# Kernel optimization log

Hardware: AMD Instinct MI355X
Metric: run time of the kernel (lower is better)

## Reference

```python
import jax, jax.numpy as jnp
import numpy as np

N = 50000      # nodes
E = 800000     # edges (avg degree 16)
IN = 256       # input feature dim
HID = 128      # hidden dim
H = 4          # heads
C = HID // H   # per-head dim = 32
L = 3          # layers


def setup_inputs() -> dict:
    key = jax.random.key(0)
    ks = jax.random.split(key, 16)
    s = 0.02
    f32 = jnp.float32
    inp = {
        "x": jax.random.normal(ks[0], (N, IN), f32),
        "edge_index": jax.random.randint(ks[1], (2, E), 0, N, dtype=jnp.int32),
        "edge_attr": jax.random.normal(ks[2], (E, 1), f32),
        "Wi": jax.random.normal(ks[3], (IN, HID), f32) * s,
        "bi": jnp.zeros((HID,), f32),
        "Wq": jax.random.normal(ks[4], (L, HID, HID), f32) * s,
        "bq": jnp.zeros((L, HID), f32),
        "Wk": jax.random.normal(ks[5], (L, HID, HID), f32) * s,
        "bk": jnp.zeros((L, HID), f32),
        "Wv": jax.random.normal(ks[6], (L, HID, HID), f32) * s,
        "bv": jnp.zeros((L, HID), f32),
        "We": jax.random.normal(ks[7], (L, 1, HID), f32) * s,      # lin_edge, no bias
        "Wskip": jax.random.normal(ks[8], (L, HID, HID), f32) * s,
        "bskip": jnp.zeros((L, HID), f32),
        "Wbeta": jax.random.normal(ks[9], (L, 3 * HID, 1), f32) * s,  # lin_beta, no bias
        "ln_g": jnp.ones((L, HID), f32),
        "ln_b": jnp.zeros((L, HID), f32),
    }
    return inp


def _layer_norm(x, g, b, eps=1e-5):
    mu = jnp.mean(x, axis=-1, keepdims=True)
    var = jnp.var(x, axis=-1, keepdims=True)
    return (x - mu) * jax.lax.rsqrt(var + eps) * g + b


def _transformer_conv(h, src, dst, edge_attr, Wq, bq, Wk, bk, Wv, bv, We, Wskip, bskip, Wbeta):
    # node-level projections [N, HID]
    q = h @ Wq + bq
    k = h @ Wk + bk
    v = h @ Wv + bv
    e = edge_attr @ We                       # [E, HID] edge embedding
    # per-edge gathered features [E, H, C]
    qi = q[dst].reshape(E, H, C)
    kj = (k[src] + e).reshape(E, H, C)
    vj = (v[src] + e).reshape(E, H, C)
    # attention logits [E, H]
    alpha = jnp.sum(qi * kj, axis=-1) / np.sqrt(C)
    # segment softmax over destination node
    amax = jax.ops.segment_max(alpha, dst, num_segments=N)   # [N, H]
    ex = jnp.exp(alpha - amax[dst])
    denom = jax.ops.segment_sum(ex, dst, num_segments=N)     # [N, H]
    attn = ex / (denom[dst] + 1e-16)                         # [E, H]
    # scatter-add aggregation -> [N, H, C] -> concat heads [N, HID]
    out = jax.ops.segment_sum(attn[..., None] * vj, dst, num_segments=N).reshape(N, HID)
    # gated skip (beta=True, root_weight=True)
    x_r = h @ Wskip + bskip
    beta = jax.nn.sigmoid(jnp.concatenate([out, x_r, out - x_r], axis=-1) @ Wbeta)  # [N, 1]
    return beta * x_r + (1.0 - beta) * out


def reference(x, edge_index, edge_attr, Wi, bi, Wq, bq, Wk, bk, Wv, bv, We, Wskip, bskip, Wbeta, ln_g, ln_b):
    src = edge_index[0]
    dst = edge_index[1]
    h = x @ Wi + bi
    for l in range(L):
        res = h
        h = _transformer_conv(h, src, dst, edge_attr,
                              Wq[l], bq[l], Wk[l], bk[l], Wv[l], bv[l],
                              We[l], Wskip[l], bskip[l], Wbeta[l])
        h = jax.nn.gelu(h, approximate=False)
        h = _layer_norm(h + res, ln_g[l], ln_b[l])
        # dropout: eval mode -> identity
    return h
```

## Files before the change

### kernel.cpp

```cpp
#include <hip/hip_runtime.h>
#include <math.h>

#define NNODES 50000
#define NEDGES 800000
#define DIN 256
#define DHID 128
#define GBLK 391
#define NBUCK 196
#define CHUNK 4096

typedef __attribute__((ext_vector_type(8))) short short8;
typedef __attribute__((ext_vector_type(4))) float f32x4;
typedef __attribute__((ext_vector_type(2))) float f32x2;

__device__ __forceinline__ unsigned short f2bf(float f) {
    unsigned u = __builtin_bit_cast(unsigned, f);
    u += 0x7fffu + ((u >> 16) & 1u);
    return (unsigned short)(u >> 16);
}
__device__ __forceinline__ float bf2f(unsigned short s) {
    return __builtin_bit_cast(float, (unsigned)s << 16);
}
__device__ __forceinline__ unsigned packbf(float a, float b) {
    return (unsigned)f2bf(a) | ((unsigned)f2bf(b) << 16);
}
__device__ __forceinline__ float dpp_xor1(float x) {
    return __builtin_bit_cast(float, __builtin_amdgcn_update_dpp(0, __builtin_bit_cast(int, x), 0xB1, 0xF, 0xF, true));
}
__device__ __forceinline__ float dpp_xor2(float x) {
    return __builtin_bit_cast(float, __builtin_amdgcn_update_dpp(0, __builtin_bit_cast(int, x), 0x4E, 0xF, 0xF, true));
}
__device__ __forceinline__ float dpp_hmirror(float x) {
    return __builtin_bit_cast(float, __builtin_amdgcn_update_dpp(0, __builtin_bit_cast(int, x), 0x141, 0xF, 0xF, true));
}
__device__ __forceinline__ float dpp_mirror(float x) {
    return __builtin_bit_cast(float, __builtin_amdgcn_update_dpp(0, __builtin_bit_cast(int, x), 0x140, 0xF, 0xF, true));
}
__device__ __forceinline__ float red16(float x) {
    x += dpp_xor1(x);
    x += dpp_xor2(x);
    x += dpp_hmirror(x);
    x += dpp_mirror(x);
    return x;
}

__global__ __launch_bounds__(256) void prep_hist(const float* __restrict__ Wi, const float* __restrict__ Wq,
                                                 const float* __restrict__ Wk, const float* __restrict__ Wv,
                                                 const float* __restrict__ Ws, unsigned short* __restrict__ Wit,
                                                 unsigned short* __restrict__ Wt3, const int* __restrict__ dst,
                                                 int* __restrict__ counts, int pb) {
    if ((int)blockIdx.x < pb) {
        int idx = blockIdx.x * 256 + threadIdx.x;
        if (idx < DHID * DIN) {
            int n = idx >> 8, kk = idx & 255;
            Wit[idx] = f2bf(Wi[kk * DHID + n]);
        }
        int idx2 = idx - DHID * DIN;
        if (idx2 >= 0 && idx2 < 3 * 512 * DHID) {
            int l = idx2 / (512 * DHID);
            int rem = idx2 - l * 512 * DHID;
            int r = rem >> 7;
            int kk = rem & 127;
            int sel = r >> 7, rl = r & 127;
            const float* srcm = sel == 0 ? Wq : sel == 1 ? Wk : sel == 2 ? Wv : Ws;
            Wt3[idx2] = f2bf(srcm[l * DHID * DHID + kk * DHID + rl]);
        }
    } else {
        int e = (blockIdx.x - pb) * 256 + threadIdx.x;
        if (e < NEDGES) atomicAdd(&counts[dst[e]], 1);
    }
}

__global__ __launch_bounds__(256) void k_scan_block(const int* __restrict__ in, int* __restrict__ out,
                                                    int* __restrict__ partials, int n, int* __restrict__ dh) {
    __shared__ int sh[256];
    __shared__ int dhist[256];
    int tid = threadIdx.x;
    int i = blockIdx.x * 256 + tid;
    int vv = (i < n) ? in[i] : 0;
    sh[tid] = vv;
    dhist[tid] = 0;
    __syncthreads();
    if (i < n) atomicAdd(&dhist[min(vv, 255)], 1);
    for (int off = 1; off < 256; off <<= 1) {
        int t = (tid >= off) ? sh[tid - off] : 0;
        __syncthreads();
        sh[tid] += t;
        __syncthreads();
    }
    if (i < n) out[i] = sh[tid];
    if (tid == 255) partials[blockIdx.x] = sh[255];
    __syncthreads();
    int hc = dhist[tid];
    if (hc) atomicAdd(&dh[tid], hc);
}

__global__ __launch_bounds__(256) void k_apply2(const int* __restrict__ partials, int* __restrict__ row_ptr, int n,
                                                int nb, const int* __restrict__ dh, int* __restrict__ dbase) {
    __shared__ int sh[256];
    int tid = threadIdx.x;
    int vv = (tid < nb) ? partials[tid] : 0;
    sh[tid] = vv;
    __syncthreads();
    for (int off = 1; off < 256; off <<= 1) {
        int t = (tid >= off) ? sh[tid - off] : 0;
        __syncthreads();
        sh[tid] += t;
        __syncthreads();
    }
    int i = blockIdx.x * 256 + tid;
    if (i < n) {
        int add = blockIdx.x ? sh[blockIdx.x - 1] : 0;
        row_ptr[i + 1] += add;
    }
    if (i == 0) row_ptr[0] = 0;
    if (blockIdx.x == 0) {
        __syncthreads();
        int c = dh[255 - tid];
        sh[tid] = c;
        __syncthreads();
        for (int off = 1; off < 256; off <<= 1) {
            int t = (tid >= off) ? sh[tid - off] : 0;
            __syncthreads();
            sh[tid] += t;
            __syncthreads();
        }
        dbase[255 - tid] = sh[tid] - c;
    }
}

__global__ __launch_bounds__(256) void perm_scatter(const int* __restrict__ counts, const int* __restrict__ dbase,
                                                    int* __restrict__ dfill, int* __restrict__ perm) {
    __shared__ int h[256], gb[256], c2[256];
    const int tid = threadIdx.x;
    int i = blockIdx.x * 256 + tid;
    int d = (i < NNODES) ? min(counts[i], 255) : -1;
    h[tid] = 0;
    c2[tid] = 0;
    __syncthreads();
    if (d >= 0) atomicAdd(&h[d], 1);
    __syncthreads();
    int c = h[tid];
    gb[tid] = c ? dbase[tid] + atomicAdd(&dfill[tid], c) : 0;
    __syncthreads();
    if (d >= 0) {
        int r = atomicAdd(&c2[d], 1);
        perm[gb[d] + r] = i;
    }
}

__global__ __launch_bounds__(256) void bin_edges(const int* __restrict__ src, const int* __restrict__ dst,
                                                 const float* __restrict__ ea, const int* __restrict__ row_ptr,
                                                 int* __restrict__ bfill, unsigned* __restrict__ brec,
                                                 unsigned char* __restrict__ bdst) {
    __shared__ int hist[NBUCK];
    __shared__ int lbase[NBUCK];
    __shared__ int gbase[NBUCK];
    __shared__ int cnt[NBUCK];
    __shared__ unsigned rec4[CHUNK];
    __shared__ unsigned char dl8[CHUNK];
    __shared__ unsigned char bk8[CHUNK];
    const int tid = threadIdx.x;
    const int e0 = blockIdx.x * CHUNK;
    const int n = min(NEDGES - e0, CHUNK);
    for (int i = tid; i < NBUCK; i += 256) hist[i] = 0;
    __syncthreads();
    for (int i = tid; i < n; i += 256) atomicAdd(&hist[dst[e0 + i] >> 8], 1);
    __syncthreads();
    if (tid == 0) {
        int run = 0;
        for (int b = 0; b < NBUCK; ++b) {
            lbase[b] = run;
            run += hist[b];
        }
    }
    __syncthreads();
    for (int b = tid; b < NBUCK; b += 256) {
        int h = hist[b];
        int off = h ? atomicAdd(&bfill[b], h) : 0;
        gbase[b] = row_ptr[b << 8] + off;
        cnt[b] = lbase[b];
    }
    __syncthreads();
    for (int i = tid; i < n; i += 256) {
        int d = dst[e0 + i];
        int b = d >> 8;
        int lp = atomicAdd(&cnt[b], 1);
        rec4[lp] = (unsigned)src[e0 + i] | ((unsigned)f2bf(ea[e0 + i]) << 16);
        dl8[lp] = (unsigned char)(d & 255);
        bk8[lp] = (unsigned char)b;
    }
    __syncthreads();
    for (int i = tid; i < n; i += 256) {
        int b = bk8[i];
        int pos = gbase[b] + (i - lbase[b]);
        brec[pos] = rec4[i];
        bdst[pos] = dl8[i];
    }
}

__global__ __launch_bounds__(256) void sort_bucket(const unsigned* __restrict__ brec,
                                                   const unsigned char* __restrict__ bdst,
                                                   const int* __restrict__ row_ptr, unsigned* __restrict__ esrc) {
    __shared__ int rp[257];
    __shared__ int cnt[256];
    const int b = blockIdx.x;
    const int d0 = b << 8;
    const int nmax = min(256, NNODES - d0);
    const int tid = threadIdx.x;
    for (int i = tid; i <= nmax; i += 256) rp[i] = row_ptr[d0 + i];
    cnt[tid] = 0;
    __syncthreads();
    const int base = rp[0], end = rp[nmax];
    for (int i = base + tid; i < end; i += 256) {
        unsigned rec = brec[i];
        int d = bdst[i];
        int rank = atomicAdd(&cnt[d], 1);
        esrc[rp[d] + rank] = rec;
    }
}

__global__ __launch_bounds__(256) void gemm_in(const float* __restrict__ A, const unsigned short* __restrict__ Wt,
                                               const float* __restrict__ bias, unsigned* __restrict__ h32, int M) {
    __shared__ short As[128 * 128];
    const int tid = threadIdx.x;
    const int lane = tid & 63;
    const int wid = tid >> 6;
    const int row0 = blockIdx.x * 128;
    const int wr = (wid & 1) * 64;
    const int wc = (wid >> 1) * 64;
    f32x4 acc[4][4] = {};
    const int srow = tid >> 1;
    const int sk = (tid & 1) * 64;
    const int grow = min(row0 + srow, M - 1);
    for (int kt = 0; kt < 2; ++kt) {
        const float* ap = A + (size_t)grow * DIN + kt * 128 + sk;
#pragma unroll
        for (int i = 0; i < 8; ++i) {
            float4 f0 = *(const float4*)(ap + i * 8);
            float4 f1 = *(const float4*)(ap + i * 8 + 4);
            short8 s;
            s[0] = f2bf(f0.x); s[1] = f2bf(f0.y); s[2] = f2bf(f0.z); s[3] = f2bf(f0.w);
            s[4] = f2bf(f1.x); s[5] = f2bf(f1.y); s[6] = f2bf(f1.z); s[7] = f2bf(f1.w);
            int g = (sk >> 3) + i;
            *(short8*)(&As[srow * 128 + ((g ^ (srow & 7)) << 3)]) = s;
        }
        __syncthreads();
#pragma unroll
        for (int ks = 0; ks < 4; ++ks) {
            short8 a[4], b[4];
#pragma unroll
            for (int m = 0; m < 4; ++m) {
                int r = wr + m * 16 + (lane & 15);
                int g = ks * 4 + (lane >> 4);
                a[m] = *(const short8*)(&As[r * 128 + ((g ^ (r & 7)) << 3)]);
            }
#pragma unroll
            for (int n = 0; n < 4; ++n) {
                int c = wc + n * 16 + (lane & 15);
                b[n] = *(const short8*)(Wt + (size_t)c * DIN + kt * 128 + ks * 32 + (lane >> 4) * 8);
            }
#pragma unroll
            for (int m = 0; m < 4; ++m)
#pragma unroll
                for (int n = 0; n < 4; ++n)
                    acc[m][n] = __builtin_amdgcn_mfma_f32_16x16x32_bf16(a[m], b[n], acc[m][n], 0, 0, 0);
        }
        __syncthreads();
    }
    float* my = ((float*)As) + wid * 1024;
    float bb[4];
#pragma unroll
    for (int n = 0; n < 4; ++n) bb[n] = bias[wc + n * 16 + (lane & 15)];
    const int rr = lane >> 2;
    const int cb = lane & 3;
#pragma unroll
    for (int m = 0; m < 4; ++m) {
#pragma unroll
        for (int n = 0; n < 4; ++n) {
            int lc = n * 16 + (lane & 15);
#pragma unroll
            for (int j = 0; j < 4; ++j) {
                int row = (lane >> 4) * 4 + j;
                my[row * 64 + (((lc >> 2) ^ (row & 7)) << 2) + (lc & 3)] = acc[m][n][j] + bb[n];
            }
        }
        float vals[16];
#pragma unroll
        for (int s = 0; s < 4; ++s) {
            int gx = (cb * 4 + s) ^ (rr & 7);
            f32x4 t4 = *(const f32x4*)(my + rr * 64 + gx * 4);
            vals[s * 4 + 0] = t4.x; vals[s * 4 + 1] = t4.y; vals[s * 4 + 2] = t4.z; vals[s * 4 + 3] = t4.w;
        }
        int grow2 = row0 + wr + m * 16 + rr;
        if (grow2 < M) {
            unsigned pk[8];
#pragma unroll
            for (int d = 0; d < 8; ++d) pk[d] = packbf(vals[2 * d], vals[2 * d + 1]);
            unsigned* op = h32 + (size_t)grow2 * 64 + (wc >> 1) + cb * 8;
            *(uint4*)op = make_uint4(pk[0], pk[1], pk[2], pk[3]);
            *(uint4*)(op + 4) = make_uint4(pk[4], pk[5], pk[6], pk[7]);
        }
    }
}

__global__ __launch_bounds__(512) void gemm_qkvs(const unsigned short* __restrict__ A,
                                                 const unsigned short* __restrict__ Wt, const float* __restrict__ bq,
                                                 const float* __restrict__ bk, const float* __restrict__ bv,
                                                 const float* __restrict__ bs, unsigned* __restrict__ q32,
                                                 unsigned* __restrict__ kv, unsigned* __restrict__ xr32, int M) {
    __shared__ short As[128 * 128];
    const int tid = threadIdx.x;
    const int lane = tid & 63;
    const int wid = tid >> 6;
    const int row0 = blockIdx.x * 128;
    const int sel = wid >> 2;
    const int wr = (wid & 1) * 64;
    const int wc = ((wid >> 1) & 1) * 64;
    f32x4 acc0[4][4] = {}, acc1[4][4] = {};
    {
        const int srow = tid >> 2;
        const int sk = (tid & 3) * 32;
        const int grow = min(row0 + srow, M - 1);
        const unsigned short* ap = A + (size_t)grow * DHID + sk;
#pragma unroll
        for (int i = 0; i < 4; ++i) {
            short8 s = *(const short8*)(ap + i * 8);
            int g = (sk >> 3) + i;
            *(short8*)(&As[srow * 128 + ((g ^ (srow & 7)) << 3)]) = s;
        }
    }
    __syncthreads();
    const int b0base = sel ? 128 : 0;
    const int b1base = sel ? 256 : 384;
#pragma unroll
    for (int ks = 0; ks < 4; ++ks) {
        short8 a[4], b0[4], b1[4];
#pragma unroll
        for (int m = 0; m < 4; ++m) {
            int r = wr + m * 16 + (lane & 15);
            int g = ks * 4 + (lane >> 4);
            a[m] = *(const short8*)(&As[r * 128 + ((g ^ (r & 7)) << 3)]);
        }
#pragma unroll
        for (int n = 0; n < 4; ++n) {
            int rb = wc + n * 16 + (lane & 15);
            b0[n] = *(const short8*)(Wt + (size_t)(b0base + rb) * DHID + ks * 32 + (lane >> 4) * 8);
            b1[n] = *(const short8*)(Wt + (size_t)(b1base + rb) * DHID + ks * 32 + (lane >> 4) * 8);
        }
#pragma unroll
        for (int m = 0; m < 4; ++m)
#pragma unroll
            for (int n = 0; n < 4; ++n) {
                acc0[m][n] = __builtin_amdgcn_mfma_f32_16x16x32_bf16(a[m], b0[n], acc0[m][n], 0, 0, 0);
                acc1[m][n] = __builtin_amdgcn_mfma_f32_16x16x32_bf16(a[m], b1[n], acc1[m][n], 0, 0, 0);
            }
    }
    __syncthreads();
    float* my = ((float*)As) + wid * 1024;
    const float* bias0 = sel ? bk : bq;
    const float* bias1 = sel ? bv : bs;
    float bb0[4], bb1[4];
#pragma unroll
    for (int n = 0; n < 4; ++n) {
        int c = wc + n * 16 + (lane & 15);
        bb0[n] = bias0[c];
        bb1[n] = bias1[c];
    }
    const int rr = lane >> 2;
    const int cb = lane & 3;
#pragma unroll
    for (int m = 0; m < 4; ++m) {
        float vals0[16], vals1[16];
#pragma unroll
        for (int n = 0; n < 4; ++n) {
            int lc = n * 16 + (lane & 15);
#pragma unroll
            for (int j = 0; j < 4; ++j) {
                int row = (lane >> 4) * 4 + j;
                my[row * 64 + (((lc >> 2) ^ (row & 7)) << 2) + (lc & 3)] = acc0[m][n][j] + bb0[n];
            }
        }
#pragma unroll
        for (int s = 0; s < 4; ++s) {
            int gx = (cb * 4 + s) ^ (rr & 7);
            f32x4 t4 = *(const f32x4*)(my + rr * 64 + gx * 4);
            vals0[s * 4 + 0] = t4.x; vals0[s * 4 + 1] = t4.y; vals0[s * 4 + 2] = t4.z; vals0[s * 4 + 3] = t4.w;
        }
#pragma unroll
        for (int n = 0; n < 4; ++n) {
            int lc = n * 16 + (lane & 15);
#pragma unroll
            for (int j = 0; j < 4; ++j) {
                int row = (lane >> 4) * 4 + j;
                my[row * 64 + (((lc >> 2) ^ (row & 7)) << 2) + (lc & 3)] = acc1[m][n][j] + bb1[n];
            }
        }
#pragma unroll
        for (int s = 0; s < 4; ++s) {
            int gx = (cb * 4 + s) ^ (rr & 7);
            f32x4 t4 = *(const f32x4*)(my + rr * 64 + gx * 4);
            vals1[s * 4 + 0] = t4.x; vals1[s * 4 + 1] = t4.y; vals1[s * 4 + 2] = t4.z; vals1[s * 4 + 3] = t4.w;
        }
        int grow2 = row0 + wr + m * 16 + rr;
        if (grow2 < M) {
            size_t obase = (size_t)grow2 * 64 + (wc >> 1) + cb * 8;
            if (sel == 0) {
                unsigned p0[8], p1[8];
#pragma unroll
                for (int d = 0; d < 8; ++d) {
                    p0[d] = packbf(vals0[2 * d], vals0[2 * d + 1]);
                    p1[d] = packbf(vals1[2 * d], vals1[2 * d + 1]);
                }
                *(uint4*)(q32 + obase) = make_uint4(p0[0], p0[1], p0[2], p0[3]);
                *(uint4*)(q32 + obase + 4) = make_uint4(p0[4], p0[5], p0[6], p0[7]);
                *(uint4*)(xr32 + obase) = make_uint4(p1[0], p1[1], p1[2], p1[3]);
                *(uint4*)(xr32 + obase + 4) = make_uint4(p1[4], p1[5], p1[6], p1[7]);
            } else {
                unsigned pk[8];
#pragma unroll
                for (int d = 0; d < 8; ++d) {
                    unsigned u = (unsigned)__builtin_amdgcn_cvt_pk_fp8_f32(vals0[2 * d], vals0[2 * d + 1], 0, false);
                    u = (unsigned)__builtin_amdgcn_cvt_pk_fp8_f32(vals1[2 * d], vals1[2 * d + 1], (int)u, true);
                    pk[d] = u;
                }
                *(uint4*)(kv + obase) = make_uint4(pk[0], pk[1], pk[2], pk[3]);
                *(uint4*)(kv + obase + 4) = make_uint4(pk[4], pk[5], pk[6], pk[7]);
            }
        }
    }
}

__global__ __launch_bounds__(256) void node_attn_fuse(const unsigned* __restrict__ q32,
                                                      const unsigned* __restrict__ kv, const unsigned* __restrict__ esrc,
                                                      const float* __restrict__ We, const int* __restrict__ row_ptr,
                                                      const int* __restrict__ perm, const unsigned* __restrict__ xr32,
                                                      const unsigned* res32, const float* __restrict__ Wb,
                                                      const float* __restrict__ lng, const float* __restrict__ lnb,
                                                      unsigned* houtb, float* houtf) {
    const int tid = threadIdx.x;
    const int lane = tid & 63;
    const int lnl = lane & 15;
    const int gbase = lane & 48;
    const int node = perm[blockIdx.x * 16 + (tid >> 4)];
    const int base = row_ptr[node], end = row_ptr[node + 1];
    const float SC = 0.25505654047688565f;
    const float THR = 8.0f;

    float qv[8], wev[8];
    {
        uint4 qw = *(const uint4*)(q32 + (size_t)node * 64 + 4 * lnl);
        unsigned qd[4] = {qw.x, qw.y, qw.z, qw.w};
#pragma unroll
        for (int t = 0; t < 4; ++t) {
            qv[2 * t] = bf2f((unsigned short)qd[t]) * SC;
            qv[2 * t + 1] = bf2f((unsigned short)(qd[t] >> 16)) * SC;
        }
        float4 wlo = *(const float4*)(We + 8 * lnl);
        float4 whi = *(const float4*)(We + 8 * lnl + 4);
        wev[0] = wlo.x; wev[1] = wlo.y; wev[2] = wlo.z; wev[3] = wlo.w;
        wev[4] = whi.x; wev[5] = whi.y; wev[6] = whi.z; wev[7] = whi.w;
    }
    float qwe;
    {
        float s = 0.f;
#pragma unroll
        for (int i = 0; i < 8; ++i) s = fmaf(qv[i], wev[i], s);
        s += dpp_xor1(s);
        s += dpp_xor2(s);
        qwe = s;
    }

    float m = -1e30f, sden = 0.f, tacc = 0.f;
    float acc[8] = {};
    const unsigned* kvp = kv + 4 * lnl;

    for (int off = 0; ; off += 16) {
        int cnt = min(end - base - off, 16);
        if (__all(cnt <= 0)) break;
        unsigned u_l = 0;
        if (lnl < cnt) u_l = esrc[base + off + lnl];
        int cm = max(cnt, 0);
        cm = max(cm, __shfl_xor(cm, 16));
        cm = max(cm, __shfl_xor(cm, 32));
        unsigned ueA[4], ueB[4];
        uint4 kwA[4], kwB[4];
#pragma unroll
        for (int s = 0; s < 4; ++s) {
            ueA[s] = (unsigned)__shfl((int)u_l, gbase + s);
            kwA[s] = *(const uint4*)(kvp + (size_t)(ueA[s] & 0xFFFFu) * 64);
        }
#pragma unroll
        for (int s = 0; s < 4; ++s) {
            ueB[s] = (unsigned)__shfl((int)u_l, gbase + 4 + s);
            kwB[s] = *(const uint4*)(kvp + (size_t)(ueB[s] & 0xFFFFu) * 64);
        }
        for (int j = 0; j < cm; j += 4) {
            float p[4], av[4];
#pragma unroll
            for (int s = 0; s < 4; ++s) {
                av[s] = bf2f((unsigned short)(ueA[s] >> 16));
                unsigned kd[4] = {kwA[s].x, kwA[s].y, kwA[s].z, kwA[s].w};
                float pp = 0.f;
#pragma unroll
                for (int t = 0; t < 4; ++t) {
                    f32x2 kk = __builtin_amdgcn_cvt_pk_f32_fp8((int)kd[t], false);
                    pp = fmaf(qv[2 * t], kk.x, pp);
                    pp = fmaf(qv[2 * t + 1], kk.y, pp);
                }
                p[s] = pp;
            }
#pragma unroll
            for (int s = 0; s < 4; ++s) {
                p[s] += dpp_xor1(p[s]);
                p[s] += dpp_xor2(p[s]);
                p[s] = fmaf(av[s], qwe, p[s]);
                p[s] = (j + s < cnt) ? p[s] : -3e38f;
            }
            float pm = fmaxf(fmaxf(p[0], p[1]), fmaxf(p[2], p[3]));
            float w[4];
            if (__any(pm - m > THR)) {
                float mn2 = fmaxf(m, pm);
                float sc = exp2f(m - mn2);
#pragma unroll
                for (int s = 0; s < 4; ++s) w[s] = exp2f(p[s] - mn2);
                sden = fmaf(sden, sc, (w[0] + w[1]) + (w[2] + w[3]));
                tacc = fmaf(tacc, sc, fmaf(w[0], av[0], w[1] * av[1]) + fmaf(w[2], av[2], w[3] * av[3]));
#pragma unroll
                for (int t = 0; t < 4; ++t) {
                    f32x2 v0 = __builtin_amdgcn_cvt_pk_f32_fp8((int)kwA[0].x, true);
                    (void)v0;
                }
#pragma unroll
                for (int i = 0; i < 8; ++i) acc[i] *= sc;
#pragma unroll
                for (int s = 0; s < 4; ++s) {
                    unsigned kd[4] = {kwA[s].x, kwA[s].y, kwA[s].z, kwA[s].w};
#pragma unroll
                    for (int t = 0; t < 4; ++t) {
                        f32x2 vv = __builtin_amdgcn_cvt_pk_f32_fp8((int)kd[t], true);
                        acc[2 * t] = fmaf(w[s], vv.x, acc[2 * t]);
                        acc[2 * t + 1] = fmaf(w[s], vv.y, acc[2 * t + 1]);
                    }
                }
                m = mn2;
            } else {
#pragma unroll
                for (int s = 0; s < 4; ++s) w[s] = exp2f(p[s] - m);
                sden += (w[0] + w[1]) + (w[2] + w[3]);
                tacc += fmaf(w[0], av[0], w[1] * av[1]) + fmaf(w[2], av[2], w[3] * av[3]);
#pragma unroll
                for (int s = 0; s < 4; ++s) {
                    unsigned kd[4] = {kwA[s].x, kwA[s].y, kwA[s].z, kwA[s].w};
#pragma unroll
                    for (int t = 0; t < 4; ++t) {
                        f32x2 vv = __builtin_amdgcn_cvt_pk_f32_fp8((int)kd[t], true);
                        acc[2 * t] = fmaf(w[s], vv.x, acc[2 * t]);
                        acc[2 * t + 1] = fmaf(w[s], vv.y, acc[2 * t + 1]);
                    }
                }
            }
#pragma unroll
            for (int s = 0; s < 4; ++s) {
                ueA[s] = ueB[s];
                kwA[s] = kwB[s];
            }
            if (j + 8 < cm) {
#pragma unroll
                for (int s = 0; s < 4; ++s) {
                    int slot = j + 8 + s;
                    slot = slot < 16 ? slot : 0;
                    ueB[s] = (unsigned)__shfl((int)u_l, gbase + slot);
                    kwB[s] = *(const uint4*)(kvp + (size_t)(ueB[s] & 0xFFFFu) * 64);
                }
            }
        }
    }

    float rden = 1.f / (sden + 1e-16f);
    float o[8];
#pragma unroll
    for (int i = 0; i < 8; ++i) o[i] = fmaf(tacc, wev[i], acc[i]) * rden;

    float x[8];
    {
        uint4 xw = *(const uint4*)(xr32 + (size_t)node * 64 + 4 * lnl);
        unsigned xd[4] = {xw.x, xw.y, xw.z, xw.w};
#pragma unroll
        for (int t = 0; t < 4; ++t) {
            x[2 * t] = bf2f((unsigned short)xd[t]);
            x[2 * t + 1] = bf2f((unsigned short)(xd[t] >> 16));
        }
    }
    float bl = 0.f;
#pragma unroll
    for (int t = 0; t < 2; ++t) {
        float4 w0 = *(const float4*)(Wb + 8 * lnl + 4 * t);
        float4 w1 = *(const float4*)(Wb + 128 + 8 * lnl + 4 * t);
        float4 w2 = *(const float4*)(Wb + 256 + 8 * lnl + 4 * t);
        bl = fmaf(o[4 * t], w0.x, bl); bl = fmaf(o[4 * t + 1], w0.y, bl);
        bl = fmaf(o[4 * t + 2], w0.z, bl); bl = fmaf(o[4 * t + 3], w0.w, bl);
        bl = fmaf(x[4 * t], w1.x, bl); bl = fmaf(x[4 * t + 1], w1.y, bl);
        bl = fmaf(x[4 * t + 2], w1.z, bl); bl = fmaf(x[4 * t + 3], w1.w, bl);
        bl = fmaf(o[4 * t] - x[4 * t], w2.x, bl); bl = fmaf(o[4 * t + 1] - x[4 * t + 1], w2.y, bl);
        bl = fmaf(o[4 * t + 2] - x[4 * t + 2], w2.z, bl); bl = fmaf(o[4 * t + 3] - x[4 * t + 3], w2.w, bl);
    }
    bl = red16(bl);
    float beta = 1.f / (1.f + __expf(-bl));
    float tpre[8];
    {
        uint4 rw = *(const uint4*)(res32 + (size_t)node * 64 + 4 * lnl);
        unsigned rd[4] = {rw.x, rw.y, rw.z, rw.w};
#pragma unroll
        for (int i = 0; i < 8; ++i) {
            float gg = beta * x[i] + (1.f - beta) * o[i];
            gg = 0.5f * gg * (1.f + erff(gg * 0.70710678118654752f));
            float rv = (i & 1) ? bf2f((unsigned short)(rd[i >> 1] >> 16)) : bf2f((unsigned short)rd[i >> 1]);
            tpre[i] = gg + rv;
        }
    }
    float su = 0.f, sq = 0.f;
#pragma unroll
    for (int i = 0; i < 8; ++i) {
        su += tpre[i];
        sq = fmaf(tpre[i], tpre[i], sq);
    }
    su = red16(su);
    sq = red16(sq);
    float mu = su * (1.f / 128.f);
    float var = sq * (1.f / 128.f) - mu * mu;
    float inv = rsqrtf(var + 1e-5f);
    float4 g0 = *(const float4*)(lng + 8 * lnl);
    float4 g1 = *(const float4*)(lng + 8 * lnl + 4);
    float4 b0 = *(const float4*)(lnb + 8 * lnl);
    float4 b1 = *(const float4*)(lnb + 8 * lnl + 4);
    float gg[8] = {g0.x, g0.y, g0.z, g0.w, g1.x, g1.y, g1.z, g1.w};
    float bb[8] = {b0.x, b0.y, b0.z, b0.w, b1.x, b1.y, b1.z, b1.w};
    float ov[8];
#pragma unroll
    for (int i = 0; i < 8; ++i) ov[i] = (tpre[i] - mu) * inv * gg[i] + bb[i];
    if (houtf) {
        float* op = houtf + (size_t)node * 128 + 8 * lnl;
        *(float4*)op = make_float4(ov[0], ov[1], ov[2], ov[3]);
        *(float4*)(op + 4) = make_float4(ov[4], ov[5], ov[6], ov[7]);
    } else {
        unsigned pk[4];
#pragma unroll
        for (int d = 0; d < 4; ++d) pk[d] = packbf(ov[2 * d], ov[2 * d + 1]);
        *(uint4*)(houtb + (size_t)node * 64 + 4 * lnl) = make_uint4(pk[0], pk[1], pk[2], pk[3]);
    }
}

extern "C" void kernel_launch(void* const* d_in, const int* in_sizes, int n_in, void* d_out, int out_size,
                              void* d_ws, size_t ws_size, hipStream_t stream) {
    const float* x = (const float*)d_in[0];
    const int* ei = (const int*)d_in[1];
    const float* ea = (const float*)d_in[2];
    const float* Wi = (const float*)d_in[3];
    const float* bi = (const float*)d_in[4];
    const float* Wq = (const float*)d_in[5];
    const float* bq = (const float*)d_in[6];
    const float* Wk = (const float*)d_in[7];
    const float* bk = (const float*)d_in[8];
    const float* Wv = (const float*)d_in[9];
    const float* bv = (const float*)d_in[10];
    const float* We = (const float*)d_in[11];
    const float* Wskip = (const float*)d_in[12];
    const float* bskip = (const float*)d_in[13];
    const float* Wbeta = (const float*)d_in[14];
    const float* lng = (const float*)d_in[15];
    const float* lnb = (const float*)d_in[16];

    const int* srcp = ei;
    const int* dstp = ei + NEDGES;

    char* p = (char*)d_ws;
    auto alloc = [&](size_t bytes) {
        void* r = (void*)p;
        p += (bytes + 255) & ~(size_t)255;
        return r;
    };
    unsigned* h32 = (unsigned*)alloc((size_t)NNODES * 64 * 4);
    unsigned* q32 = (unsigned*)alloc((size_t)NNODES * 64 * 4);
    unsigned* xr32 = (unsigned*)alloc((size_t)NNODES * 64 * 4);
    unsigned* kv = (unsigned*)alloc((size_t)NNODES * 64 * 4);
    unsigned short* Wit = (unsigned short*)alloc((size_t)DHID * DIN * 2);
    unsigned short* Wt3 = (unsigned short*)alloc((size_t)3 * 512 * DHID * 2);
    int* counts = (int*)alloc((size_t)(NNODES + 768) * 4);
    int* bfill = counts + NNODES;
    int* dh = bfill + 256;
    int* dfill = dh + 256;
    int* dbase = (int*)alloc(256 * 4);
    int* perm = (int*)alloc((size_t)NNODES * 4);
    int* row_ptr = (int*)alloc((size_t)(NNODES + 1) * 4);
    unsigned* esrc = (unsigned*)alloc((size_t)NEDGES * 4);
    unsigned* brec = (unsigned*)alloc((size_t)NEDGES * 4);
    unsigned char* bdst = (unsigned char*)alloc((size_t)NEDGES);
    int* partials = (int*)alloc(256 * 4);

    const int EB = (NEDGES + 255) / 256;
    const int NB = (NNODES + 255) / 256;
    const int WB = NNODES / 16;
    const int PB = (DHID * DIN + 3 * 512 * DHID + 255) / 256;
    const int AB = (NEDGES + CHUNK - 1) / CHUNK;

    hipMemsetAsync(counts, 0, (size_t)(NNODES + 768) * 4, stream);
    prep_hist<<<PB + EB, 256, 0, stream>>>(Wi, Wq, Wk, Wv, Wskip, Wit, Wt3, dstp, counts, PB);
    gemm_in<<<GBLK, 256, 0, stream>>>(x, Wit, bi, h32, NNODES);
    k_scan_block<<<NB, 256, 0, stream>>>(counts, row_ptr + 1, partials, NNODES, dh);
    k_apply2<<<NB, 256, 0, stream>>>(partials, row_ptr, NNODES, NB, dh, dbase);
    perm_scatter<<<NB, 256, 0, stream>>>(counts, dbase, dfill, perm);
    bin_edges<<<AB, 256, 0, stream>>>(srcp, dstp, ea, row_ptr, bfill, brec, bdst);
    sort_bucket<<<NBUCK, 256, 0, stream>>>(brec, bdst, row_ptr, esrc);

    for (int l = 0; l < 3; ++l) {
        const size_t bo = (size_t)l * 128;
        gemm_qkvs<<<GBLK, 512, 0, stream>>>((const unsigned short*)h32, Wt3 + (size_t)l * 512 * DHID, bq + bo, bk + bo,
                                            bv + bo, bskip + bo, q32, kv, xr32, NNODES);
        node_attn_fuse<<<WB, 256, 0, stream>>>(q32, kv, esrc, We + bo, row_ptr, perm, xr32, h32,
                                               Wbeta + (size_t)l * 384, lng + bo, lnb + bo, h32,
                                               (l == 2) ? (float*)d_out : nullptr);
    }
}
```

Baseline: 311.1 us.

## Split online softmax into two independent streams and merge perm/bin kernels

The attention loop now processes 8 edges per iteration as two independent online-softmax accumulators (X and Y), each with its own running max, denominator and accumulator, merged at the end. Loads for the next 8 edges are issued before the current ones are computed, which lengthens the prefetch distance and breaks the serial dependency on a single running max. Separately, the perm_scatter and bin_edges kernels are fused into one launch that branches on block index, saving a launch. The cost is higher register pressure from doubled accumulators and prefetch buffers, which could lower occupancy.

```diff
diff --git a/kernel.cpp b/kernel.cpp
--- a/kernel.cpp
+++ b/kernel.cpp
@@ -129,30 +129,12 @@
     }
 }
 
-__global__ __launch_bounds__(256) void perm_scatter(const int* __restrict__ counts, const int* __restrict__ dbase,
-                                                    int* __restrict__ dfill, int* __restrict__ perm) {
-    __shared__ int h[256], gb[256], c2[256];
-    const int tid = threadIdx.x;
-    int i = blockIdx.x * 256 + tid;
-    int d = (i < NNODES) ? min(counts[i], 255) : -1;
-    h[tid] = 0;
-    c2[tid] = 0;
-    __syncthreads();
-    if (d >= 0) atomicAdd(&h[d], 1);
-    __syncthreads();
-    int c = h[tid];
-    gb[tid] = c ? dbase[tid] + atomicAdd(&dfill[tid], c) : 0;
-    __syncthreads();
-    if (d >= 0) {
-        int r = atomicAdd(&c2[d], 1);
-        perm[gb[d] + r] = i;
-    }
-}
-
-__global__ __launch_bounds__(256) void bin_edges(const int* __restrict__ src, const int* __restrict__ dst,
-                                                 const float* __restrict__ ea, const int* __restrict__ row_ptr,
-                                                 int* __restrict__ bfill, unsigned* __restrict__ brec,
-                                                 unsigned char* __restrict__ bdst) {
+__global__ __launch_bounds__(256) void perm_bin(const int* __restrict__ counts, const int* __restrict__ dbase,
+                                                int* __restrict__ dfill, int* __restrict__ perm,
+                                                const int* __restrict__ src, const int* __restrict__ dst,
+                                                const float* __restrict__ ea, const int* __restrict__ row_ptr,
+                                                int* __restrict__ bfill, unsigned* __restrict__ brec,
+                                                unsigned char* __restrict__ bdst, int nb) {
     __shared__ int hist[NBUCK];
     __shared__ int lbase[NBUCK];
     __shared__ int gbase[NBUCK];
@@ -161,7 +143,27 @@
     __shared__ unsigned char dl8[CHUNK];
     __shared__ unsigned char bk8[CHUNK];
     const int tid = threadIdx.x;
-    const int e0 = blockIdx.x * CHUNK;
+    if ((int)blockIdx.x < nb) {
+        int* h = (int*)rec4;
+        int* gb = h + 256;
+        int* c2 = gb + 256;
+        int i = blockIdx.x * 256 + tid;
+        int d = (i < NNODES) ? min(counts[i], 255) : -1;
+        h[tid] = 0;
+        c2[tid] = 0;
+        __syncthreads();
+        if (d >= 0) atomicAdd(&h[d], 1);
+        __syncthreads();
+        int c = h[tid];
+        gb[tid] = c ? dbase[tid] + atomicAdd(&dfill[tid], c) : 0;
+        __syncthreads();
+        if (d >= 0) {
+            int r = atomicAdd(&c2[d], 1);
+            perm[gb[d] + r] = i;
+        }
+        return;
+    }
+    const int e0 = (blockIdx.x - nb) * CHUNK;
     const int n = min(NEDGES - e0, CHUNK);
     for (int i = tid; i < NBUCK; i += 256) hist[i] = 0;
     __syncthreads();
@@ -471,11 +473,11 @@
         qwe = s;
     }
 
-    float m = -1e30f, sden = 0.f, tacc = 0.f;
-    float acc[8] = {};
+    float mX = -1e30f, sdX = 0.f, taX = 0.f, accX[8] = {};
+    float mY = -1e30f, sdY = 0.f, taY = 0.f, accY[8] = {};
     const unsigned* kvp = kv + 4 * lnl;
 
-    for (int off = 0; ; off += 16) {
+    for (int off = 0;; off += 16) {
         int cnt = min(end - base - off, 16);
         if (__all(cnt <= 0)) break;
         unsigned u_l = 0;
@@ -484,103 +486,155 @@
         cm = max(cm, __shfl_xor(cm, 16));
         cm = max(cm, __shfl_xor(cm, 32));
         unsigned ueA[4], ueB[4];
-        uint4 kwA[4], kwB[4];
+        uint4 QA[4], QB[4];
 #pragma unroll
         for (int s = 0; s < 4; ++s) {
             ueA[s] = (unsigned)__shfl((int)u_l, gbase + s);
-            kwA[s] = *(const uint4*)(kvp + (size_t)(ueA[s] & 0xFFFFu) * 64);
+            QA[s] = *(const uint4*)(kvp + (size_t)(ueA[s] & 0xFFFFu) * 64);
         }
 #pragma unroll
         for (int s = 0; s < 4; ++s) {
             ueB[s] = (unsigned)__shfl((int)u_l, gbase + 4 + s);
-            kwB[s] = *(const uint4*)(kvp + (size_t)(ueB[s] & 0xFFFFu) * 64);
-        }
-        for (int j = 0; j < cm; j += 4) {
-            float p[4], av[4];
-#pragma unroll
-            for (int s = 0; s < 4; ++s) {
-                av[s] = bf2f((unsigned short)(ueA[s] >> 16));
-                unsigned kd[4] = {kwA[s].x, kwA[s].y, kwA[s].z, kwA[s].w};
-                float pp = 0.f;
-#pragma unroll
-                for (int t = 0; t < 4; ++t) {
-                    f32x2 kk = __builtin_amdgcn_cvt_pk_f32_fp8((int)kd[t], false);
-                    pp = fmaf(qv[2 * t], kk.x, pp);
-                    pp = fmaf(qv[2 * t + 1], kk.y, pp);
-                }
-                p[s] = pp;
-            }
-#pragma unroll
-            for (int s = 0; s < 4; ++s) {
-                p[s] += dpp_xor1(p[s]);
-                p[s] += dpp_xor2(p[s]);
-                p[s] = fmaf(av[s], qwe, p[s]);
-                p[s] = (j + s < cnt) ? p[s] : -3e38f;
-            }
-            float pm = fmaxf(fmaxf(p[0], p[1]), fmaxf(p[2], p[3]));
-            float w[4];
-            if (__any(pm - m > THR)) {
-                float mn2 = fmaxf(m, pm);
-                float sc = exp2f(m - mn2);
-#pragma unroll
-                for (int s = 0; s < 4; ++s) w[s] = exp2f(p[s] - mn2);
-                sden = fmaf(sden, sc, (w[0] + w[1]) + (w[2] + w[3]));
-                tacc = fmaf(tacc, sc, fmaf(w[0], av[0], w[1] * av[1]) + fmaf(w[2], av[2], w[3] * av[3]));
-#pragma unroll
-                for (int t = 0; t < 4; ++t) {
-                    f32x2 v0 = __builtin_amdgcn_cvt_pk_f32_fp8((int)kwA[0].x, true);
-                    (void)v0;
-                }
-#pragma unroll
-                for (int i = 0; i < 8; ++i) acc[i] *= sc;
-#pragma unroll
-                for (int s = 0; s < 4; ++s) {
-                    unsigned kd[4] = {kwA[s].x, kwA[s].y, kwA[s].z, kwA[s].w};
+            QB[s] = *(const uint4*)(kvp + (size_t)(ueB[s] & 0xFFFFu) * 64);
+        }
+        for (int j = 0; j < cm; j += 8) {
+            unsigned ueA2[4], ueB2[4];
+            uint4 QA2[4], QB2[4];
+            bool more = (j + 8 < cm);
+            if (more) {
+#pragma unroll
+                for (int s = 0; s < 4; ++s) {
+                    ueA2[s] = (unsigned)__shfl((int)u_l, gbase + j + 8 + s);
+                    QA2[s] = *(const uint4*)(kvp + (size_t)(ueA2[s] & 0xFFFFu) * 64);
+                }
+#pragma unroll
+                for (int s = 0; s < 4; ++s) {
+                    ueB2[s] = (unsigned)__shfl((int)u_l, gbase + j + 12 + s);
+                    QB2[s] = *(const uint4*)(kvp + (size_t)(ueB2[s] & 0xFFFFu) * 64);
+                }
+            }
+            {
+                float p[4], av[4], w[4];
+#pragma unroll
+                for (int s = 0; s < 4; ++s) {
+                    av[s] = bf2f((unsigned short)(ueA[s] >> 16));
+                    unsigned kd[4] = {QA[s].x, QA[s].y, QA[s].z, QA[s].w};
+                    float pp = 0.f;
+#pragma unroll
+                    for (int t = 0; t < 4; ++t) {
+                        f32x2 kk = __builtin_amdgcn_cvt_pk_f32_fp8((int)kd[t], false);
+                        pp = fmaf(qv[2 * t], kk.x, pp);
+                        pp = fmaf(qv[2 * t + 1], kk.y, pp);
+                    }
+                    p[s] = pp;
+                }
+#pragma unroll
+                for (int s = 0; s < 4; ++s) {
+                    p[s] += dpp_xor1(p[s]);
+                    p[s] += dpp_xor2(p[s]);
+                    p[s] = fmaf(av[s], qwe, p[s]);
+                    p[s] = (j + s < cnt) ? p[s] : -3e38f;
+                }
+                float pm = fmaxf(fmaxf(p[0], p[1]), fmaxf(p[2], p[3]));
+                if (__any(pm - mX > THR)) {
+                    float mn2 = fmaxf(mX, pm);
+                    float sc = exp2f(mX - mn2);
+#pragma unroll
+                    for (int s = 0; s < 4; ++s) w[s] = exp2f(p[s] - mn2);
+                    sdX = fmaf(sdX, sc, (w[0] + w[1]) + (w[2] + w[3]));
+                    taX = fmaf(taX, sc, fmaf(w[0], av[0], w[1] * av[1]) + fmaf(w[2], av[2], w[3] * av[3]));
+#pragma unroll
+                    for (int i = 0; i < 8; ++i) accX[i] *= sc;
+                    mX = mn2;
+                } else {
+#pragma unroll
+                    for (int s = 0; s < 4; ++s) w[s] = exp2f(p[s] - mX);
+                    sdX += (w[0] + w[1]) + (w[2] + w[3]);
+                    taX += fmaf(w[0], av[0], w[1] * av[1]) + fmaf(w[2], av[2], w[3] * av[3]);
+                }
+#pragma unroll
+                for (int s = 0; s < 4; ++s) {
+                    unsigned kd[4] = {QA[s].x, QA[s].y, QA[s].z, QA[s].w};
 #pragma unroll
                     for (int t = 0; t < 4; ++t) {
                         f32x2 vv = __builtin_amdgcn_cvt_pk_f32_fp8((int)kd[t], true);
-                        acc[2 * t] = fmaf(w[s], vv.x, acc[2 * t]);
-                        acc[2 * t + 1] = fmaf(w[s], vv.y, acc[2 * t + 1]);
+                        accX[2 * t] = fmaf(w[s], vv.x, accX[2 * t]);
+                        accX[2 * t + 1] = fmaf(w[s], vv.y, accX[2 * t + 1]);
                     }
                 }
-                m = mn2;
-            } else {
-#pragma unroll
-                for (int s = 0; s < 4; ++s) w[s] = exp2f(p[s] - m);
-                sden += (w[0] + w[1]) + (w[2] + w[3]);
-                tacc += fmaf(w[0], av[0], w[1] * av[1]) + fmaf(w[2], av[2], w[3] * av[3]);
-#pragma unroll
-                for (int s = 0; s < 4; ++s) {
-                    unsigned kd[4] = {kwA[s].x, kwA[s].y, kwA[s].z, kwA[s].w};
+            }
+            {
+                float p[4], av[4], w[4];
+#pragma unroll
+                for (int s = 0; s < 4; ++s) {
+                    av[s] = bf2f((unsigned short)(ueB[s] >> 16));
+                    unsigned kd[4] = {QB[s].x, QB[s].y, QB[s].z, QB[s].w};
+                    float pp = 0.f;
+#pragma unroll
+                    for (int t = 0; t < 4; ++t) {
+                        f32x2 kk = __builtin_amdgcn_cvt_pk_f32_fp8((int)kd[t], false);
+                        pp = fmaf(qv[2 * t], kk.x, pp);
+                        pp = fmaf(qv[2 * t + 1], kk.y, pp);
+                    }
+                    p[s] = pp;
+                }
+#pragma unroll
+                for (int s = 0; s < 4; ++s) {
+                    p[s] += dpp_xor1(p[s]);
+                    p[s] += dpp_xor2(p[s]);
+                    p[s] = fmaf(av[s], qwe, p[s]);
+                    p[s] = (j + 4 + s < cnt) ? p[s] : -3e38f;
+                }
+                float pm = fmaxf(fmaxf(p[0], p[1]), fmaxf(p[2], p[3]));
+                if (__any(pm - mY > THR)) {
+                    float mn2 = fmaxf(mY, pm);
+                    float sc = exp2f(mY - mn2);
+#pragma unroll
+                    for (int s = 0; s < 4; ++s) w[s] = exp2f(p[s] - mn2);
+                    sdY = fmaf(sdY, sc, (w[0] + w[1]) + (w[2] + w[3]));
+                    taY = fmaf(taY, sc, fmaf(w[0], av[0], w[1] * av[1]) + fmaf(w[2], av[2], w[3] * av[3]));
+#pragma unroll
+                    for (int i = 0; i < 8; ++i) accY[i] *= sc;
+                    mY = mn2;
+                } else {
+#pragma unroll
+                    for (int s = 0; s < 4; ++s) w[s] = exp2f(p[s] - mY);
+                    sdY += (w[0] + w[1]) + (w[2] + w[3]);
+                    taY += fmaf(w[0], av[0], w[1] * av[1]) + fmaf(w[2], av[2], w[3] * av[3]);
+                }
+#pragma unroll
+                for (int s = 0; s < 4; ++s) {
+                    unsigned kd[4] = {QB[s].x, QB[s].y, QB[s].z, QB[s].w};
 #pragma unroll
                     for (int t = 0; t < 4; ++t) {
                         f32x2 vv = __builtin_amdgcn_cvt_pk_f32_fp8((int)kd[t], true);
-                        acc[2 * t] = fmaf(w[s], vv.x, acc[2 * t]);
-                        acc[2 * t + 1] = fmaf(w[s], vv.y, acc[2 * t + 1]);
+                        accY[2 * t] = fmaf(w[s], vv.x, accY[2 * t]);
+                        accY[2 * t + 1] = fmaf(w[s], vv.y, accY[2 * t + 1]);
                     }
                 }
             }
-#pragma unroll
-            for (int s = 0; s < 4; ++s) {
-                ueA[s] = ueB[s];
-                kwA[s] = kwB[s];
-            }
-            if (j + 8 < cm) {
-#pragma unroll
-                for (int s = 0; s < 4; ++s) {
-                    int slot = j + 8 + s;
-                    slot = slot < 16 ? slot : 0;
-                    ueB[s] = (unsigned)__shfl((int)u_l, gbase + slot);
-                    kwB[s] = *(const uint4*)(kvp + (size_t)(ueB[s] & 0xFFFFu) * 64);
-                }
-            }
-        }
-    }
-
-    float rden = 1.f / (sden + 1e-16f);
+            if (more) {
+#pragma unroll
+                for (int s = 0; s < 4; ++s) {
+                    ueA[s] = ueA2[s]; QA[s] = QA2[s];
+                    ueB[s] = ueB2[s]; QB[s] = QB2[s];
+                }
+            }
+        }
+    }
+
+    {
+        float mn = fmaxf(mX, mY);
+        float sa = exp2f(mX - mn), sb = exp2f(mY - mn);
+        sdX = sdX * sa + sdY * sb;
+        taX = taX * sa + taY * sb;
+#pragma unroll
+        for (int i = 0; i < 8; ++i) accX[i] = accX[i] * sa + accY[i] * sb;
+    }
+    float rden = 1.f / (sdX + 1e-16f);
     float o[8];
 #pragma unroll
-    for (int i = 0; i < 8; ++i) o[i] = fmaf(tacc, wev[i], acc[i]) * rden;
+    for (int i = 0; i < 8; ++i) o[i] = fmaf(taX, wev[i], accX[i]) * rden;
 
     float x[8];
     {
@@ -709,8 +763,7 @@
     gemm_in<<<GBLK, 256, 0, stream>>>(x, Wit, bi, h32, NNODES);
     k_scan_block<<<NB, 256, 0, stream>>>(counts, row_ptr + 1, partials, NNODES, dh);
     k_apply2<<<NB, 256, 0, stream>>>(partials, row_ptr, NNODES, NB, dh, dbase);
-    perm_scatter<<<NB, 256, 0, stream>>>(counts, dbase, dfill, perm);
-    bin_edges<<<AB, 256, 0, stream>>>(srcp, dstp, ea, row_ptr, bfill, brec, bdst);
+    perm_bin<<<NB + AB, 256, 0, stream>>>(counts, dbase, dfill, perm, srcp, dstp, ea, row_ptr, bfill, brec, bdst, NB);
     sort_bucket<<<NBUCK, 256, 0, stream>>>(brec, bdst, row_ptr, esrc);
 
     for (int l = 0; l < 3; ++l) {
```

Measured after the change: 336.3 us. 1.08x slower.
